# Kernel optimization log

Hardware: AMD Instinct MI355X
Metric: run time of the kernel (lower is better)

Reference implementation:

```python
import jax, jax.numpy as jnp
import numpy as np

N_NODES = 50000
N_EDGES = 800000
EPS = 0.1

def setup_inputs() -> dict:
    key = jax.random.key(0)
    ks = jax.random.split(key, 6)
    x = jax.random.normal(ks[0], (N_NODES, 256), dtype=jnp.float32)
    edge_index = jax.random.randint(ks[1], (2, N_EDGES), 0, N_NODES, dtype=jnp.int64)
    W1 = jax.random.normal(ks[2], (256, 64), dtype=jnp.float32) * (1.0 / np.sqrt(256))
    b1 = jnp.zeros((64,), dtype=jnp.float32)
    att = jax.random.normal(ks[3], (2, 1, 64), dtype=jnp.float32) * (1.0 / np.sqrt(64))
    W2 = jax.random.normal(ks[4], (64, 16), dtype=jnp.float32) * (1.0 / np.sqrt(64))
    b2 = jnp.zeros((16,), dtype=jnp.float32)
    return {"x": x, "edge_index": edge_index, "W1": W1, "b1": b1, "att": att, "W2": W2, "b2": b2}

def _fagcn_conv(x, row, col, norm, att_l, eps):
    # message: norm * x_j gathered at source (row), scatter-add to target (col)
    msg = norm[:, None] * x[row]                      # [E_tot, H]
    x_l = jax.ops.segment_sum(msg, col, num_segments=N_NODES)  # low-pass
    x_h = -eps * x_l                                   # high-pass message = -eps * low message
    gate = jax.nn.sigmoid(jnp.sum(x * att_l, axis=-1, keepdims=True))  # [N,1]
    return gate * x_l + (1.0 - gate) * x_h

def reference(x, edge_index, W1, b1, att, W2, b2):
    # add self loops once (same edge set is reused by every layer)
    loops = jnp.arange(N_NODES, dtype=edge_index.dtype)
    row = jnp.concatenate([edge_index[0], loops])
    col = jnp.concatenate([edge_index[1], loops])
    deg = jax.ops.segment_sum(jnp.ones_like(col, dtype=x.dtype), col, num_segments=N_NODES)
    dinv = jnp.where(deg > 0, jax.lax.rsqrt(jnp.maximum(deg, 1e-30)), 0.0)
    norm = dinv[row] * dinv[col]                       # [E_tot]
    # eval mode: dropout is identity
    h = jax.nn.relu(x @ W1 + b1)                       # [N, H]
    for l in range(att.shape[0]):
        h = _fagcn_conv(h, row, col, norm, att[l], EPS)
    return h @ W2 + b2                                 # [N, out]
```

## Files before the change

### kernel.cpp

```cpp
#include <hip/hip_runtime.h>
#include <math.h>

#define N_FEAT_IN 256
#define N_HID 64
#define N_OUT 16
#define EPS 0.1f

typedef short bf16x8 __attribute__((ext_vector_type(8)));
typedef float f32x4 __attribute__((ext_vector_type(4)));

__device__ inline uint pack2(ushort a, ushort b) { return (uint)a | ((uint)b << 16); }

__device__ inline ushort bf16_rne(float x) {
    uint b = __float_as_uint(x);
    b += 0x7fff + ((b >> 16) & 1);
    return (ushort)(b >> 16);
}

__device__ inline float blo(uint u) { return __uint_as_float(u << 16); }
__device__ inline float bhi(uint u) { return __uint_as_float(u & 0xffff0000u); }

__device__ inline void split_bf16(float x, ushort& hi, ushort& lo) {
    uint b = __float_as_uint(x);
    hi = (ushort)(b >> 16);
    float xl = x - __uint_as_float(b & 0xffff0000u);
    lo = (ushort)(__float_as_uint(xl) >> 16);
}


__global__ void zero_int(int* __restrict__ p, int n) {
    int i = blockIdx.x * blockDim.x + threadIdx.x;
    if (i < n) p[i] = 0;
}


__global__ void hist_rank(const int* __restrict__ col, const int* __restrict__ row,
                          int* __restrict__ cnt, uint* __restrict__ rr, int E) {
    int e = blockIdx.x * blockDim.x + threadIdx.x;
    if (e < E) {
        int r = atomicAdd(&cnt[col[e]], 1);
        rr[e] = ((uint)r << 16) | (uint)row[e];
    }
}


__global__ void scan_chunks(const int* __restrict__ cnt, int* __restrict__ rowptr,
                            int* __restrict__ partial, float* __restrict__ dinv, int N) {
    __shared__ int sm[256];
    int tid = threadIdx.x;
    int gid = blockIdx.x * 256 + tid;
    int v = (gid < N) ? cnt[gid] : 0;
    sm[tid] = v;
    __syncthreads();
#pragma unroll
    for (int off = 1; off < 256; off <<= 1) {
        int add = (tid >= off) ? sm[tid - off] : 0;
        __syncthreads();
        sm[tid] += add;
        __syncthreads();
    }
    if (gid < N) {
        rowptr[gid] = sm[tid] - v;
        dinv[gid] = rsqrtf(1.0f + (float)v);
    }
    if (tid == 255) partial[blockIdx.x] = sm[255];
}


__global__ void scan_finish(int* __restrict__ rowptr, const int* __restrict__ partial,
                            int N, int E, int nchunks) {
    __shared__ int sm[256];
    int tid = threadIdx.x;
    sm[tid] = (tid < nchunks) ? partial[tid] : 0;
    __syncthreads();
#pragma unroll
    for (int off = 1; off < 256; off <<= 1) {
        int add = (tid >= off) ? sm[tid - off] : 0;
        __syncthreads();
        sm[tid] += add;
        __syncthreads();
    }
    int boff = (blockIdx.x == 0) ? 0 : sm[blockIdx.x - 1];
    __syncthreads();
    int gid = blockIdx.x * 256 + tid;
    if (gid < N) rowptr[gid] += boff;
    if (gid == 0) rowptr[N] = E;
}


__global__ void csr_scatter_part(const int* __restrict__ col, const uint* __restrict__ rr,
                                 const int* __restrict__ rowptr,
                                 ushort* __restrict__ srcidx, int E, int rangeSz) {
    int r = blockIdx.x & 7;
    int nsl = gridDim.x >> 3;
    int s = blockIdx.x >> 3;
    int lo = r * rangeSz;
    int hi = lo + rangeSz;
    int stride = nsl * blockDim.x;
    for (int e = s * blockDim.x + threadIdx.x; e < E; e += stride) {
        int c = col[e];
        if (c >= lo && c < hi) {
            uint v = rr[e];
            srcidx[rowptr[c] + (v >> 16)] = (ushort)(v & 0xffffu);
        }
    }
}


__global__ __launch_bounds__(256) void gemm1_mfma(const float* __restrict__ x,
                                                  const float* __restrict__ W1,
                                                  const float* __restrict__ b1,
                                                  const float* __restrict__ dinv,
                                                  uint* __restrict__ AsOut,
                                                  int MB, int totalWaves) {
    __shared__ uint4 wh_lds[2048];
    __shared__ uint4 wl_lds[2048];
    int tid = threadIdx.x;
    for (int e = tid; e < 2048; e += 256) {
        int ks = e >> 8;
        int rem = e & 255;
        int nt = rem >> 6;
        int ln = rem & 63;
        int k0 = ks * 32 + ((ln >> 4) << 3);
        int colw = nt * 16 + (ln & 15);
        ushort hi[8], lo[8];
#pragma unroll
        for (int i = 0; i < 8; ++i) {
            float v = W1[(k0 + i) * 64 + colw];
            split_bf16(v, hi[i], lo[i]);
        }
        wh_lds[e] = make_uint4(pack2(hi[0], hi[1]), pack2(hi[2], hi[3]),
                               pack2(hi[4], hi[5]), pack2(hi[6], hi[7]));
        wl_lds[e] = make_uint4(pack2(lo[0], lo[1]), pack2(lo[2], lo[3]),
                               pack2(lo[4], lo[5]), pack2(lo[6], lo[7]));
    }
    __syncthreads();

    int lane = tid & 63;
    int m = lane & 15;
    int kg = lane >> 4;
    int wid = blockIdx.x * 4 + (tid >> 6);
    const bf16x8* whf = reinterpret_cast<const bf16x8*>(wh_lds);
    const bf16x8* wlf = reinterpret_cast<const bf16x8*>(wl_lds);
    float bias[4];
#pragma unroll
    for (int nt = 0; nt < 4; ++nt) bias[nt] = b1[nt * 16 + m];

    auto load_tile = [&](float4* dst, int mbv) {
        const float4* xr = reinterpret_cast<const float4*>(x) +
                           (size_t)(mbv * 16 + m) * 64 + kg * 2;
#pragma unroll
        for (int ks = 0; ks < 8; ++ks) {
            dst[2 * ks]     = xr[ks * 8];
            dst[2 * ks + 1] = xr[ks * 8 + 1];
        }
    };

    int mb = wid;
    if (mb >= MB) return;
    float4 xv[16], xn[16];
    load_tile(xv, mb);

    while (true) {
        int mbn = mb + totalWaves;
        bool has_next = (mbn < MB);
        if (has_next) load_tile(xn, mbn);

        f32x4 acc[4] = {{0.f,0.f,0.f,0.f},{0.f,0.f,0.f,0.f},
                        {0.f,0.f,0.f,0.f},{0.f,0.f,0.f,0.f}};
#pragma unroll
        for (int ks = 0; ks < 8; ++ks) {
            float4 a0 = xv[2 * ks];
            float4 a1 = xv[2 * ks + 1];
            float f[8] = {a0.x, a0.y, a0.z, a0.w, a1.x, a1.y, a1.z, a1.w};
            bf16x8 ah, al;
#pragma unroll
            for (int i = 0; i < 8; ++i) {
                ushort hu, lu;
                split_bf16(f[i], hu, lu);
                ah[i] = (short)hu;
                al[i] = (short)lu;
            }
#pragma unroll
            for (int nt = 0; nt < 4; ++nt) {
                bf16x8 wh = whf[(ks * 4 + nt) * 64 + lane];
                bf16x8 wl = wlf[(ks * 4 + nt) * 64 + lane];
                acc[nt] = __builtin_amdgcn_mfma_f32_16x16x32_bf16(ah, wh, acc[nt], 0, 0, 0);
                acc[nt] = __builtin_amdgcn_mfma_f32_16x16x32_bf16(al, wh, acc[nt], 0, 0, 0);
                acc[nt] = __builtin_amdgcn_mfma_f32_16x16x32_bf16(ah, wl, acc[nt], 0, 0, 0);
            }
        }

        int r0 = mb * 16 + kg * 4;
        float dr[4];
#pragma unroll
        for (int j = 0; j < 4; ++j) dr[j] = dinv[r0 + j];
#pragma unroll
        for (int nt = 0; nt < 4; ++nt) {
#pragma unroll
            for (int j = 0; j < 4; ++j) {
                float v = fmaxf(acc[nt][j] + bias[nt], 0.0f) * dr[j];
                float p = __shfl_xor(v, 1, 64);
                if ((m & 1) == 0) {
                    uint u = pack2(bf16_rne(v), bf16_rne(p));
                    AsOut[(size_t)(r0 + j) * 32 + ((nt * 16 + m) >> 1)] = u;
                }
            }
        }

        if (!has_next) break;
#pragma unroll
        for (int u = 0; u < 16; ++u) xv[u] = xn[u];
        mb = mbn;
    }
}


template <bool LAST>
__global__ __launch_bounds__(256) void fagcn_layer(
    const uint4* __restrict__ As4, uint4* __restrict__ Out4,
    const float* __restrict__ dinv, const int* __restrict__ rowptr,
    const ushort* __restrict__ src, const float* __restrict__ att_l,
    const float* __restrict__ W2, const float* __restrict__ b2,
    float* __restrict__ out, int N) {
    __shared__ float W2s[64 * 16];
    __shared__ float hL[32 * 68];
    int tid = threadIdx.x;
    if (LAST) {
        for (int e = tid; e < 64 * 16; e += 256) W2s[e] = W2[e];
        __syncthreads();
    }
    int sub = tid & 7;
    int lnode = tid >> 3;
    int i = blockIdx.x * 32 + lnode;
    if (i >= N) i = N - 1;

    int start = rowptr[i];
    int end = rowptr[i + 1];
    const uint4* Ab = As4 + sub;
    uint4 su = Ab[(size_t)i * 8];
    float s0 = blo(su.x), s1 = bhi(su.x), s2 = blo(su.y), s3 = bhi(su.y);
    float s4 = blo(su.z), s5 = bhi(su.z), s6 = blo(su.w), s7 = bhi(su.w);

    float aA0=0.f,aA1=0.f,aA2=0.f,aA3=0.f,aA4=0.f,aA5=0.f,aA6=0.f,aA7=0.f;
    float aB0=0.f,aB1=0.f,aB2=0.f,aB3=0.f,aB4=0.f,aB5=0.f,aB6=0.f,aB7=0.f;
    int j = start;
    for (; j + 3 < end; j += 4) {
        int e0 = src[j];
        int e1 = src[j + 1];
        int e2 = src[j + 2];
        int e3 = src[j + 3];
        uint4 u0 = Ab[(size_t)e0 * 8];
        uint4 u1 = Ab[(size_t)e1 * 8];
        uint4 u2 = Ab[(size_t)e2 * 8];
        uint4 u3 = Ab[(size_t)e3 * 8];
        aA0 += blo(u0.x); aA1 += bhi(u0.x); aA2 += blo(u0.y); aA3 += bhi(u0.y);
        aA4 += blo(u0.z); aA5 += bhi(u0.z); aA6 += blo(u0.w); aA7 += bhi(u0.w);
        aB0 += blo(u1.x); aB1 += bhi(u1.x); aB2 += blo(u1.y); aB3 += bhi(u1.y);
        aB4 += blo(u1.z); aB5 += bhi(u1.z); aB6 += blo(u1.w); aB7 += bhi(u1.w);
        aA0 += blo(u2.x); aA1 += bhi(u2.x); aA2 += blo(u2.y); aA3 += bhi(u2.y);
        aA4 += blo(u2.z); aA5 += bhi(u2.z); aA6 += blo(u2.w); aA7 += bhi(u2.w);
        aB0 += blo(u3.x); aB1 += bhi(u3.x); aB2 += blo(u3.y); aB3 += bhi(u3.y);
        aB4 += blo(u3.z); aB5 += bhi(u3.z); aB6 += blo(u3.w); aB7 += bhi(u3.w);
    }
    for (; j < end; ++j) {
        int s = src[j];
        uint4 u = Ab[(size_t)s * 8];
        aA0 += blo(u.x); aA1 += bhi(u.x); aA2 += blo(u.y); aA3 += bhi(u.y);
        aA4 += blo(u.z); aA5 += bhi(u.z); aA6 += blo(u.w); aA7 += bhi(u.w);
    }
    float c0 = aA0 + aB0, c1 = aA1 + aB1, c2 = aA2 + aB2, c3 = aA3 + aB3;
    float c4 = aA4 + aB4, c5 = aA5 + aB5, c6 = aA6 + aB6, c7 = aA7 + aB7;

    float d = dinv[i];
    float4 at0 = reinterpret_cast<const float4*>(att_l)[2 * sub];
    float4 at1 = reinterpret_cast<const float4*>(att_l)[2 * sub + 1];
    float prod = s0 * at0.x + s1 * at0.y + s2 * at0.z + s3 * at0.w +
                 s4 * at1.x + s5 * at1.y + s6 * at1.z + s7 * at1.w;
#pragma unroll
    for (int off = 4; off > 0; off >>= 1)
        prod += __shfl_xor(prod, off, 64);
    float gate = 1.0f / (1.0f + expf(-prod / d));
    float factor = gate * (1.0f + EPS) - EPS;
    float df = d * factor;
    float h0 = df * (c0 + s0), h1 = df * (c1 + s1);
    float h2 = df * (c2 + s2), h3 = df * (c3 + s3);
    float h4 = df * (c4 + s4), h5 = df * (c5 + s5);
    float h6 = df * (c6 + s6), h7 = df * (c7 + s7);

    if (!LAST) {
        Out4[(size_t)i * 8 + sub] =
            make_uint4(pack2(bf16_rne(d * h0), bf16_rne(d * h1)),
                       pack2(bf16_rne(d * h2), bf16_rne(d * h3)),
                       pack2(bf16_rne(d * h4), bf16_rne(d * h5)),
                       pack2(bf16_rne(d * h6), bf16_rne(d * h7)));
    } else {
        float4* hrow4 = reinterpret_cast<float4*>(&hL[lnode * 68]);
        hrow4[2 * sub]     = make_float4(h0, h1, h2, h3);
        hrow4[2 * sub + 1] = make_float4(h4, h5, h6, h7);
        __syncthreads();
        const float4* h4p = reinterpret_cast<const float4*>(&hL[lnode * 68]);
        float accA = b2[sub];
        float accB = b2[sub + 8];
#pragma unroll
        for (int k4 = 0; k4 < 16; ++k4) {
            float4 hv = h4p[k4];
            int k = 4 * k4;
            accA = fmaf(hv.x, W2s[(k + 0) * 16 + sub], accA);
            accB = fmaf(hv.x, W2s[(k + 0) * 16 + sub + 8], accB);
            accA = fmaf(hv.y, W2s[(k + 1) * 16 + sub], accA);
            accB = fmaf(hv.y, W2s[(k + 1) * 16 + sub + 8], accB);
            accA = fmaf(hv.z, W2s[(k + 2) * 16 + sub], accA);
            accB = fmaf(hv.z, W2s[(k + 2) * 16 + sub + 8], accB);
            accA = fmaf(hv.w, W2s[(k + 3) * 16 + sub], accA);
            accB = fmaf(hv.w, W2s[(k + 3) * 16 + sub + 8], accB);
        }
        out[(size_t)i * 16 + sub] = accA;
        out[(size_t)i * 16 + sub + 8] = accB;
    }
}

extern "C" void kernel_launch(void* const* d_in, const int* in_sizes, int n_in,
                              void* d_out, int out_size, void* d_ws, size_t ws_size,
                              hipStream_t stream) {
    const float* x   = (const float*)d_in[0];
    const int*   ei  = (const int*)d_in[1];
    const float* W1  = (const float*)d_in[2];
    const float* b1  = (const float*)d_in[3];
    const float* att = (const float*)d_in[4];
    const float* W2  = (const float*)d_in[5];
    const float* b2  = (const float*)d_in[6];
    float* out = (float*)d_out;

    const int N = in_sizes[0] / N_FEAT_IN;
    const int E = in_sizes[1] / 2;
    const int L = in_sizes[4] / N_HID;

    const int* row = ei;
    const int* col = ei + E;

    char* wp = (char*)d_ws;
    auto alloc = [&](size_t bytes) -> char* {
        char* p = wp;
        wp += (bytes + 255) & ~(size_t)255;
        return p;
    };
    float*  dinv    = (float*)alloc((size_t)N * 4);
    int*    cnt     = (int*)alloc((size_t)N * 4);
    int*    rowptr  = (int*)alloc((size_t)(N + 1) * 4);
    uint*   rr      = (uint*)alloc((size_t)E * 4);
    int*    partial = (int*)alloc(256 * 4);
    ushort* srcidx  = (ushort*)alloc((size_t)E * 2);
    uint*   AsA     = (uint*)alloc((size_t)N * 32 * 4);
    uint*   AsB     = (uint*)alloc((size_t)N * 32 * 4);

    const int TB = 256;
    const int nchunks = (N + TB - 1) / TB;
    const int rangeSz = (N + 7) / 8;
    const int PART_GRID = 1024;

    zero_int<<<(N + TB - 1) / TB, TB, 0, stream>>>(cnt, N);
    hist_rank<<<(E + TB - 1) / TB, TB, 0, stream>>>(col, row, cnt, rr, E);
    scan_chunks<<<nchunks, TB, 0, stream>>>(cnt, rowptr, partial, dinv, N);
    scan_finish<<<nchunks, TB, 0, stream>>>(rowptr, partial, N, E, nchunks);
    csr_scatter_part<<<PART_GRID, TB, 0, stream>>>(col, rr, rowptr, srcidx, E, rangeSz);

    {
        const int blocks = 512;
        const int MB = N / 16;
        gemm1_mfma<<<blocks, TB, 0, stream>>>(x, W1, b1, dinv, AsA, MB, blocks * 4);
    }

    {
        int grid = (N + 31) / 32;
        uint4* A = (uint4*)AsA;
        uint4* B = (uint4*)AsB;
        for (int l = 0; l < L; ++l) {
            const float* att_l = att + (size_t)l * N_HID;
            if (l == L - 1) {
                fagcn_layer<true><<<grid, TB, 0, stream>>>(
                    A, B, dinv, rowptr, srcidx, att_l, W2, b2, out, N);
            } else {
                fagcn_layer<false><<<grid, TB, 0, stream>>>(
                    A, B, dinv, rowptr, srcidx, att_l, W2, b2, out, N);
                uint4* tmp = A; A = B; B = tmp;
            }
        }
    }
}
```

Measured before the change: 127.2 us.

## Share x tile across block via swizzled LDS, split output columns across waves

The first GEMM now stages each 16-row x tile in LDS with an XOR swizzle, cooperatively loaded by the whole block. Each of the four waves computes one 16-column slice instead of one wave doing all 64 columns per tile. This removes the per-wave register double-buffer of 32 float4s and spreads MFMA work across waves. In exchange it adds block-wide barriers per tile, drops software prefetch of the next tile, and makes all four waves redo the bf16 hi/lo split of the same x data.

```diff
diff --git a/kernel.cpp b/kernel.cpp
--- a/kernel.cpp
+++ b/kernel.cpp
@@ -112,9 +112,10 @@
                                                   const float* __restrict__ b1,
                                                   const float* __restrict__ dinv,
                                                   uint* __restrict__ AsOut,
-                                                  int MB, int totalWaves) {
+                                                  int MB) {
     __shared__ uint4 wh_lds[2048];
     __shared__ uint4 wl_lds[2048];
+    __shared__ float4 xt4[1024];
     int tid = threadIdx.x;
     for (int e = tid; e < 2048; e += 256) {
         int ks = e >> 8;
@@ -134,44 +135,33 @@
         wl_lds[e] = make_uint4(pack2(lo[0], lo[1]), pack2(lo[2], lo[3]),
                                pack2(lo[4], lo[5]), pack2(lo[6], lo[7]));
     }
-    __syncthreads();
 
     int lane = tid & 63;
     int m = lane & 15;
-    int kg = lane >> 4;
-    int wid = blockIdx.x * 4 + (tid >> 6);
+    int g = lane >> 4;
+    int w = tid >> 6;
     const bf16x8* whf = reinterpret_cast<const bf16x8*>(wh_lds);
     const bf16x8* wlf = reinterpret_cast<const bf16x8*>(wl_lds);
-    float bias[4];
-#pragma unroll
-    for (int nt = 0; nt < 4; ++nt) bias[nt] = b1[nt * 16 + m];
-
-    auto load_tile = [&](float4* dst, int mbv) {
-        const float4* xr = reinterpret_cast<const float4*>(x) +
-                           (size_t)(mbv * 16 + m) * 64 + kg * 2;
+    float bias = b1[w * 16 + m];
+    int swz = m & 7;
+
+    for (int mb = blockIdx.x; mb < MB; mb += gridDim.x) {
+        __syncthreads();
+        const float4* xg = reinterpret_cast<const float4*>(x) + (size_t)mb * 1024;
+#pragma unroll
+        for (int t = 0; t < 4; ++t) {
+            int F = t * 256 + tid;
+            int r = F >> 6, c4 = F & 63;
+            xt4[r * 64 + (c4 ^ (r & 7))] = xg[F];
+        }
+        __syncthreads();
+
+        f32x4 acc = {0.f, 0.f, 0.f, 0.f};
 #pragma unroll
         for (int ks = 0; ks < 8; ++ks) {
-            dst[2 * ks]     = xr[ks * 8];
-            dst[2 * ks + 1] = xr[ks * 8 + 1];
-        }
-    };
-
-    int mb = wid;
-    if (mb >= MB) return;
-    float4 xv[16], xn[16];
-    load_tile(xv, mb);
-
-    while (true) {
-        int mbn = mb + totalWaves;
-        bool has_next = (mbn < MB);
-        if (has_next) load_tile(xn, mbn);
-
-        f32x4 acc[4] = {{0.f,0.f,0.f,0.f},{0.f,0.f,0.f,0.f},
-                        {0.f,0.f,0.f,0.f},{0.f,0.f,0.f,0.f}};
-#pragma unroll
-        for (int ks = 0; ks < 8; ++ks) {
-            float4 a0 = xv[2 * ks];
-            float4 a1 = xv[2 * ks + 1];
+            int c4 = ks * 8 + g * 2;
+            float4 a0 = xt4[m * 64 + ((c4) ^ swz)];
+            float4 a1 = xt4[m * 64 + ((c4 + 1) ^ swz)];
             float f[8] = {a0.x, a0.y, a0.z, a0.w, a1.x, a1.y, a1.z, a1.w};
             bf16x8 ah, al;
 #pragma unroll
@@ -181,37 +171,23 @@
                 ah[i] = (short)hu;
                 al[i] = (short)lu;
             }
-#pragma unroll
-            for (int nt = 0; nt < 4; ++nt) {
-                bf16x8 wh = whf[(ks * 4 + nt) * 64 + lane];
-                bf16x8 wl = wlf[(ks * 4 + nt) * 64 + lane];
-                acc[nt] = __builtin_amdgcn_mfma_f32_16x16x32_bf16(ah, wh, acc[nt], 0, 0, 0);
-                acc[nt] = __builtin_amdgcn_mfma_f32_16x16x32_bf16(al, wh, acc[nt], 0, 0, 0);
-                acc[nt] = __builtin_amdgcn_mfma_f32_16x16x32_bf16(ah, wl, acc[nt], 0, 0, 0);
+            bf16x8 wh = whf[(ks * 4 + w) * 64 + lane];
+            bf16x8 wl = wlf[(ks * 4 + w) * 64 + lane];
+            acc = __builtin_amdgcn_mfma_f32_16x16x32_bf16(ah, wh, acc, 0, 0, 0);
+            acc = __builtin_amdgcn_mfma_f32_16x16x32_bf16(al, wh, acc, 0, 0, 0);
+            acc = __builtin_amdgcn_mfma_f32_16x16x32_bf16(ah, wl, acc, 0, 0, 0);
+        }
+
+        int r0 = mb * 16 + g * 4;
+#pragma unroll
+        for (int j = 0; j < 4; ++j) {
+            float v = fmaxf(acc[j] + bias, 0.0f) * dinv[r0 + j];
+            float p = __shfl_xor(v, 1, 64);
+            if ((m & 1) == 0) {
+                uint u = pack2(bf16_rne(v), bf16_rne(p));
+                AsOut[(size_t)(r0 + j) * 32 + ((w * 16 + m) >> 1)] = u;
             }
         }
-
-        int r0 = mb * 16 + kg * 4;
-        float dr[4];
-#pragma unroll
-        for (int j = 0; j < 4; ++j) dr[j] = dinv[r0 + j];
-#pragma unroll
-        for (int nt = 0; nt < 4; ++nt) {
-#pragma unroll
-            for (int j = 0; j < 4; ++j) {
-                float v = fmaxf(acc[nt][j] + bias[nt], 0.0f) * dr[j];
-                float p = __shfl_xor(v, 1, 64);
-                if ((m & 1) == 0) {
-                    uint u = pack2(bf16_rne(v), bf16_rne(p));
-                    AsOut[(size_t)(r0 + j) * 32 + ((nt * 16 + m) >> 1)] = u;
-                }
-            }
-        }
-
-        if (!has_next) break;
-#pragma unroll
-        for (int u = 0; u < 16; ++u) xv[u] = xn[u];
-        mb = mbn;
     }
 }
 
@@ -368,7 +344,7 @@
     {
         const int blocks = 512;
         const int MB = N / 16;
-        gemm1_mfma<<<blocks, TB, 0, stream>>>(x, W1, b1, dinv, AsA, MB, blocks * 4);
+        gemm1_mfma<<<blocks, TB, 0, stream>>>(x, W1, b1, dinv, AsA, MB);
     }
 
     {
```

After: 123.1 us (median of 2 runs). 1.03x faster.
